# Optimization experiments

Hardware: AMD Instinct MI355X
Metric: run time of the kernel (lower is better)

Reference implementation:

```python
import jax, jax.numpy as jnp
import numpy as np

N, M, D, K = 50000, 32, 128, 8
DELTA_D = D // K
EPS = 1e-12  # torch F.normalize eps


def _normalize(v, axis):
    nrm = jnp.linalg.norm(v, axis=axis, keepdims=True)
    return v / jnp.maximum(nrm, EPS)


def setup_inputs() -> dict:
    key = jax.random.key(0)
    k1, k2 = jax.random.split(key)
    x = jax.random.normal(k1, (N, D), dtype=jnp.float32)
    neighbors = jax.random.randint(k2, (N * M,), 0, N + 1, dtype=jnp.int64)
    return {"x": x, "neighbors": neighbors, "max_iter": 6}


def reference(x, neighbors, max_iter):
    n, d = x.shape
    m = neighbors.shape[0] // n
    k, delta_d = K, DELTA_D
    # per-capsule L2 normalize input features
    x = _normalize(x.reshape(n, k, delta_d), axis=2).reshape(n, d)
    # append zero row for padding index n, gather neighbor features
    z = jnp.concatenate([x, jnp.zeros((1, d), dtype=x.dtype)], axis=0)
    z = z[neighbors].reshape(n, m, k, delta_d)
    x_c = x.reshape(n, k, delta_d)
    u = None
    for it in range(max_iter):
        if u is None:
            p = jnp.zeros((n, m, k), dtype=x.dtype)
        else:
            p = jnp.einsum('nmkd,nkd->nmk', z, u)
        p = jax.nn.softmax(p, axis=2)
        u = jnp.einsum('nmkd,nmk->nkd', z, p) + x_c
        if it < max_iter - 1:
            u = _normalize(u, axis=2)
    return u.reshape(n, d)
```

## Files before the change

### kernel.cpp

```cpp
#include <hip/hip_runtime.h>
#include <math.h>


constexpr int NROWS = 50000;
constexpr int MN = 32;
constexpr int DDIM = 128;
constexpr float FEPS2 = 1e-24f;
constexpr float LOG2E = 1.44269504088896340736f;

#if __has_builtin(__builtin_amdgcn_rcpf)
__device__ __forceinline__ float fast_rcp(float v) { return __builtin_amdgcn_rcpf(v); }
#else
__device__ __forceinline__ float fast_rcp(float v) { return __frcp_rn(v); }
#endif
#if __has_builtin(__builtin_amdgcn_rsqf)
__device__ __forceinline__ float fast_rsq(float v) { return __builtin_amdgcn_rsqf(v); }
#else
__device__ __forceinline__ float fast_rsq(float v) { return rsqrtf(v); }
#endif
#if __has_builtin(__builtin_amdgcn_exp2f)
__device__ __forceinline__ float fast_exp2(float v) { return __builtin_amdgcn_exp2f(v); }
#else
__device__ __forceinline__ float fast_exp2(float v) { return exp2f(v); }
#endif

template <int CTRL>
__device__ __forceinline__ float dpp_add(float v) {
    int r = __builtin_amdgcn_update_dpp(0, __builtin_bit_cast(int, v), CTRL, 0xF, 0xF, true);
    return v + __builtin_bit_cast(float, r);
}

__device__ __forceinline__ void load16(float (&dst)[16], const float* __restrict__ p) {
    const float4* q = reinterpret_cast<const float4*>(p);
#pragma unroll
    for (int i = 0; i < 4; ++i) {
        float4 v = q[i];
        dst[4 * i + 0] = v.x; dst[4 * i + 1] = v.y;
        dst[4 * i + 2] = v.z; dst[4 * i + 3] = v.w;
    }
}

__device__ __forceinline__ void normalize16(float (&v)[16]) {
    float a = v[0] * v[0], b = v[1] * v[1];
#pragma unroll
    for (int d = 2; d < 16; d += 2) {
        a = fmaf(v[d], v[d], a);
        b = fmaf(v[d + 1], v[d + 1], b);
    }
    float iv = fast_rsq(fmaxf(a + b, FEPS2));
#pragma unroll
    for (int d = 0; d < 16; ++d) v[d] *= iv;
}

__device__ __forceinline__ void butterfly8(float (&u)[16]) {
#pragma unroll
    for (int d = 0; d < 16; ++d) u[d] = dpp_add<0xB1>(u[d]);
#pragma unroll
    for (int d = 0; d < 16; ++d) u[d] = dpp_add<0x4E>(u[d]);
#pragma unroll
    for (int d = 0; d < 16; ++d) u[d] += __shfl_xor(u[d], 4);
}

__device__ __forceinline__ float inv_norm_log2e(const float (&u)[16]) {
    float a = u[0] * u[0], b = u[1] * u[1];
#pragma unroll
    for (int d = 2; d < 16; d += 2) {
        a = fmaf(u[d], u[d], a);
        b = fmaf(u[d + 1], u[d + 1], b);
    }
    return fast_rsq(fmaxf(a + b, FEPS2)) * LOG2E;
}

__global__ __launch_bounds__(256) void norm_kernel(const float* __restrict__ x,
                                                   float* __restrict__ xn) {
    int t = blockIdx.x * 256 + threadIdx.x;
    constexpr int TOTAL = (NROWS + 1) * (DDIM / 4);
    if (t >= TOTAL) return;
    int n = t >> 5;
    float4 v = make_float4(0.f, 0.f, 0.f, 0.f);
    if (n < NROWS) v = reinterpret_cast<const float4*>(x)[t];
    float ss = v.x * v.x;
    ss = fmaf(v.y, v.y, ss);
    ss = fmaf(v.z, v.z, ss);
    ss = fmaf(v.w, v.w, ss);
    ss = dpp_add<0xB1>(ss);
    ss = dpp_add<0x4E>(ss);
    float iv = fast_rsq(fmaxf(ss, FEPS2));
    v.x *= iv; v.y *= iv; v.z *= iv; v.w *= iv;
    reinterpret_cast<float4*>(xn)[t] = v;
}

template <bool PRENORM>
__global__ __launch_bounds__(256, 4) void routing_kernel(const float* __restrict__ xsrc,
                                                         const int* __restrict__ nbr,
                                                         float* __restrict__ out) {
    const int lane = threadIdx.x & 63;
    const int n = blockIdx.x * 4 + (threadIdx.x >> 6);
    const int j = lane & 7;
    const int k = lane >> 3;

    float xc8[16];
    load16(xc8, xsrc + n * DDIM + k * 16);
    if (!PRENORM) normalize16(xc8);
#pragma unroll
    for (int d = 0; d < 16; ++d) xc8[d] *= 0.125f;

    float z[4][16];
    {
        const int* __restrict__ nrow = nbr + n * MN;
        int idx[4];
#pragma unroll
        for (int t = 0; t < 4; ++t) idx[t] = nrow[j + 8 * t];
#pragma unroll
        for (int t = 0; t < 4; ++t) {
            if (PRENORM) {
                load16(z[t], xsrc + idx[t] * DDIM + k * 16);
            } else {
                if (idx[t] < NROWS) {
                    load16(z[t], xsrc + idx[t] * DDIM + k * 16);
                    normalize16(z[t]);
                } else {
#pragma unroll
                    for (int d = 0; d < 16; ++d) z[t][d] = 0.f;
                }
            }
        }
    }

    float u[16];
#pragma unroll
    for (int d = 0; d < 16; ++d) {
        float a = fmaf(z[0][d], 0.125f, xc8[d]);
        a = fmaf(z[1][d], 0.125f, a);
        a = fmaf(z[2][d], 0.125f, a);
        a = fmaf(z[3][d], 0.125f, a);
        u[d] = a;
    }
    butterfly8(u);
    float c = inv_norm_log2e(u);

#pragma unroll
    for (int it = 1; it < 6; ++it) {
        float pn[4];
#pragma unroll
        for (int t = 0; t < 4; ++t) {
            float a = z[t][0] * u[0], b = z[t][1] * u[1];
#pragma unroll
            for (int d = 2; d < 16; d += 2) {
                a = fmaf(z[t][d], u[d], a);
                b = fmaf(z[t][d + 1], u[d + 1], b);
            }
            float e = fast_exp2((a + b) * c);
            float s = dpp_add<0x128>(e);
            s += __shfl_xor(s, 16);
            s += __shfl_xor(s, 32);
            pn[t] = e * fast_rcp(s);
        }
#pragma unroll
        for (int d = 0; d < 16; ++d) {
            float a = fmaf(z[0][d], pn[0], xc8[d]);
            a = fmaf(z[1][d], pn[1], a);
            a = fmaf(z[2][d], pn[2], a);
            a = fmaf(z[3][d], pn[3], a);
            u[d] = a;
        }
        butterfly8(u);
        if (it < 5) c = inv_norm_log2e(u);
    }

    float w0 = u[0], w1 = u[1];
#pragma unroll
    for (int d = 1; d < 8; ++d) {
        if (j == d) { w0 = u[2 * d]; w1 = u[2 * d + 1]; }
    }
    *reinterpret_cast<float2*>(out + n * DDIM + 2 * lane) = make_float2(w0, w1);
}

extern "C" void kernel_launch(void* const* d_in, const int* in_sizes, int n_in,
                              void* d_out, int out_size, void* d_ws, size_t ws_size,
                              hipStream_t stream) {
    const float* x = (const float*)d_in[0];
    const int* nbr = (const int*)d_in[1];
    float* out = (float*)d_out;

    const size_t need = (size_t)(NROWS + 1) * DDIM * sizeof(float);
    if (ws_size >= need) {
        float* xn = (float*)d_ws;
        constexpr int TOTAL = (NROWS + 1) * (DDIM / 4);
        norm_kernel<<<(TOTAL + 255) / 256, 256, 0, stream>>>(x, xn);
        routing_kernel<true><<<NROWS / 4, 256, 0, stream>>>(xn, nbr, out);
    } else {
        routing_kernel<false><<<NROWS / 4, 256, 0, stream>>>(x, nbr, out);
    }
}
```

Measured before the change: 203.4 us.

## Store normalized features in fp16 and use packed fp16 dot products

The normalized feature table is now written as fp16, halving the bytes moved by the random neighbor gather. The routing kernel keeps the neighbor vectors in packed half2 registers, computes the agreement dot products with fdot2, and accumulates the weighted sums in fp32. Fewer registers allow the launch-bounds occupancy hint to rise from 4 to 5. The cost is reduced precision in the gathered features and routing logits, which may push results past tolerance.

```diff
diff --git a/kernel.cpp b/kernel.cpp
--- a/kernel.cpp
+++ b/kernel.cpp
@@ -8,6 +8,12 @@
 constexpr float FEPS2 = 1e-24f;
 constexpr float LOG2E = 1.44269504088896340736f;
 
+typedef _Float16 h2 __attribute__((ext_vector_type(2)));
+typedef _Float16 h8 __attribute__((ext_vector_type(8)));
+typedef __fp16 fp16x2 __attribute__((ext_vector_type(2)));
+
+union H8Cast { h8 v; h2 p[4]; };
+
 #if __has_builtin(__builtin_amdgcn_rcpf)
 __device__ __forceinline__ float fast_rcp(float v) { return __builtin_amdgcn_rcpf(v); }
 #else
@@ -30,6 +36,27 @@
     return v + __builtin_bit_cast(float, r);
 }
 
+__device__ __forceinline__ float hdot2(h2 a, h2 b, float c) {
+#if __has_builtin(__builtin_amdgcn_fdot2)
+    return __builtin_amdgcn_fdot2(__builtin_bit_cast(fp16x2, a),
+                                  __builtin_bit_cast(fp16x2, b), c, false);
+#else
+    return fmaf((float)a[0], (float)b[0], fmaf((float)a[1], (float)b[1], c));
+#endif
+}
+
+__device__ __forceinline__ h2 pack2(float a, float b) {
+#if __has_builtin(__builtin_amdgcn_cvt_pkrtz)
+    return __builtin_bit_cast(h2, __builtin_amdgcn_cvt_pkrtz(a, b));
+#else
+    h2 r; r[0] = (_Float16)a; r[1] = (_Float16)b; return r;
+#endif
+}
+
+__device__ __forceinline__ float mixfma(_Float16 h, float s, float acc) {
+    return fmaf((float)h, s, acc);
+}
+
 __device__ __forceinline__ void load16(float (&dst)[16], const float* __restrict__ p) {
     const float4* q = reinterpret_cast<const float4*>(p);
 #pragma unroll
@@ -72,7 +99,7 @@
 }
 
 __global__ __launch_bounds__(256) void norm_kernel(const float* __restrict__ x,
-                                                   float* __restrict__ xn) {
+                                                   _Float16* __restrict__ xn) {
     int t = blockIdx.x * 256 + threadIdx.x;
     constexpr int TOTAL = (NROWS + 1) * (DDIM / 4);
     if (t >= TOTAL) return;
@@ -86,12 +113,16 @@
     ss = dpp_add<0xB1>(ss);
     ss = dpp_add<0x4E>(ss);
     float iv = fast_rsq(fmaxf(ss, FEPS2));
-    v.x *= iv; v.y *= iv; v.z *= iv; v.w *= iv;
-    reinterpret_cast<float4*>(xn)[t] = v;
+    h2 lo = pack2(v.x * iv, v.y * iv);
+    h2 hi = pack2(v.z * iv, v.w * iv);
+    float2 w;
+    w.x = __builtin_bit_cast(float, lo);
+    w.y = __builtin_bit_cast(float, hi);
+    reinterpret_cast<float2*>(xn)[t] = w;
 }
 
 template <bool PRENORM>
-__global__ __launch_bounds__(256, 4) void routing_kernel(const float* __restrict__ xsrc,
+__global__ __launch_bounds__(256, 5) void routing_kernel(const void* __restrict__ xsrc,
                                                          const int* __restrict__ nbr,
                                                          float* __restrict__ out) {
     const int lane = threadIdx.x & 63;
@@ -99,56 +130,83 @@
     const int j = lane & 7;
     const int k = lane >> 3;
 
-    float xc8[16];
-    load16(xc8, xsrc + n * DDIM + k * 16);
-    if (!PRENORM) normalize16(xc8);
-#pragma unroll
-    for (int d = 0; d < 16; ++d) xc8[d] *= 0.125f;
-
-    float z[4][16];
-    {
-        const int* __restrict__ nrow = nbr + n * MN;
-        int idx[4];
-#pragma unroll
-        for (int t = 0; t < 4; ++t) idx[t] = nrow[j + 8 * t];
+    const int* __restrict__ nrow = nbr + n * MN;
+    int idx[4];
+#pragma unroll
+    for (int t = 0; t < 4; ++t) idx[t] = nrow[j + 8 * t];
+
+    h2 z[4][8];
+    h2 xch[8];
+
+    if constexpr (PRENORM) {
+        const _Float16* xh = (const _Float16*)xsrc;
+        {
+            const h8* p = (const h8*)(xh + (size_t)n * DDIM + k * 16);
+            H8Cast a, b; a.v = p[0]; b.v = p[1];
+#pragma unroll
+            for (int q = 0; q < 4; ++q) { xch[q] = a.p[q]; xch[q + 4] = b.p[q]; }
+        }
 #pragma unroll
         for (int t = 0; t < 4; ++t) {
-            if (PRENORM) {
-                load16(z[t], xsrc + idx[t] * DDIM + k * 16);
+            const h8* p = (const h8*)(xh + (size_t)idx[t] * DDIM + k * 16);
+            H8Cast a, b; a.v = p[0]; b.v = p[1];
+#pragma unroll
+            for (int q = 0; q < 4; ++q) { z[t][q] = a.p[q]; z[t][q + 4] = b.p[q]; }
+        }
+    } else {
+        const float* xf = (const float*)xsrc;
+        float tmp[16];
+        load16(tmp, xf + (size_t)n * DDIM + k * 16);
+        normalize16(tmp);
+#pragma unroll
+        for (int q = 0; q < 8; ++q) xch[q] = pack2(tmp[2 * q], tmp[2 * q + 1]);
+#pragma unroll
+        for (int t = 0; t < 4; ++t) {
+            if (idx[t] < NROWS) {
+                load16(tmp, xf + (size_t)idx[t] * DDIM + k * 16);
+                normalize16(tmp);
             } else {
-                if (idx[t] < NROWS) {
-                    load16(z[t], xsrc + idx[t] * DDIM + k * 16);
-                    normalize16(z[t]);
-                } else {
-#pragma unroll
-                    for (int d = 0; d < 16; ++d) z[t][d] = 0.f;
-                }
+#pragma unroll
+                for (int d = 0; d < 16; ++d) tmp[d] = 0.f;
             }
-        }
-    }
+#pragma unroll
+            for (int q = 0; q < 8; ++q) z[t][q] = pack2(tmp[2 * q], tmp[2 * q + 1]);
+        }
+    }
+
+#pragma unroll
+    for (int q = 0; q < 8; ++q) xch[q] = xch[q] * (_Float16)0.125f;
 
     float u[16];
 #pragma unroll
-    for (int d = 0; d < 16; ++d) {
-        float a = fmaf(z[0][d], 0.125f, xc8[d]);
-        a = fmaf(z[1][d], 0.125f, a);
-        a = fmaf(z[2][d], 0.125f, a);
-        a = fmaf(z[3][d], 0.125f, a);
-        u[d] = a;
+    for (int q = 0; q < 8; ++q) {
+#pragma unroll
+        for (int g = 0; g < 2; ++g) {
+            float acc = (float)xch[q][g];
+            acc = mixfma(z[0][q][g], 0.125f, acc);
+            acc = mixfma(z[1][q][g], 0.125f, acc);
+            acc = mixfma(z[2][q][g], 0.125f, acc);
+            acc = mixfma(z[3][q][g], 0.125f, acc);
+            u[2 * q + g] = acc;
+        }
     }
     butterfly8(u);
     float c = inv_norm_log2e(u);
+    h2 uh[8];
+#pragma unroll
+    for (int q = 0; q < 8; ++q) uh[q] = pack2(u[2 * q], u[2 * q + 1]);
 
 #pragma unroll
     for (int it = 1; it < 6; ++it) {
         float pn[4];
 #pragma unroll
         for (int t = 0; t < 4; ++t) {
-            float a = z[t][0] * u[0], b = z[t][1] * u[1];
-#pragma unroll
-            for (int d = 2; d < 16; d += 2) {
-                a = fmaf(z[t][d], u[d], a);
-                b = fmaf(z[t][d + 1], u[d + 1], b);
+            float a = hdot2(z[t][0], uh[0], 0.f);
+            float b = hdot2(z[t][1], uh[1], 0.f);
+#pragma unroll
+            for (int q = 2; q < 8; q += 2) {
+                a = hdot2(z[t][q], uh[q], a);
+                b = hdot2(z[t][q + 1], uh[q + 1], b);
             }
             float e = fast_exp2((a + b) * c);
             float s = dpp_add<0x128>(e);
@@ -157,15 +215,23 @@
             pn[t] = e * fast_rcp(s);
         }
 #pragma unroll
-        for (int d = 0; d < 16; ++d) {
-            float a = fmaf(z[0][d], pn[0], xc8[d]);
-            a = fmaf(z[1][d], pn[1], a);
-            a = fmaf(z[2][d], pn[2], a);
-            a = fmaf(z[3][d], pn[3], a);
-            u[d] = a;
+        for (int q = 0; q < 8; ++q) {
+#pragma unroll
+            for (int g = 0; g < 2; ++g) {
+                float acc = (float)xch[q][g];
+                acc = mixfma(z[0][q][g], pn[0], acc);
+                acc = mixfma(z[1][q][g], pn[1], acc);
+                acc = mixfma(z[2][q][g], pn[2], acc);
+                acc = mixfma(z[3][q][g], pn[3], acc);
+                u[2 * q + g] = acc;
+            }
         }
         butterfly8(u);
-        if (it < 5) c = inv_norm_log2e(u);
+        if (it < 5) {
+            c = inv_norm_log2e(u);
+#pragma unroll
+            for (int q = 0; q < 8; ++q) uh[q] = pack2(u[2 * q], u[2 * q + 1]);
+        }
     }
 
     float w0 = u[0], w1 = u[1];
@@ -173,7 +239,7 @@
     for (int d = 1; d < 8; ++d) {
         if (j == d) { w0 = u[2 * d]; w1 = u[2 * d + 1]; }
     }
-    *reinterpret_cast<float2*>(out + n * DDIM + 2 * lane) = make_float2(w0, w1);
+    *reinterpret_cast<float2*>(out + (size_t)n * DDIM + 2 * lane) = make_float2(w0, w1);
 }
 
 extern "C" void kernel_launch(void* const* d_in, const int* in_sizes, int n_in,
@@ -183,9 +249,9 @@
     const int* nbr = (const int*)d_in[1];
     float* out = (float*)d_out;
 
-    const size_t need = (size_t)(NROWS + 1) * DDIM * sizeof(float);
+    const size_t need = (size_t)(NROWS + 1) * DDIM * sizeof(_Float16);
     if (ws_size >= need) {
-        float* xn = (float*)d_ws;
+        _Float16* xn = (_Float16*)d_ws;
         constexpr int TOTAL = (NROWS + 1) * (DDIM / 4);
         norm_kernel<<<(TOTAL + 255) / 256, 256, 0, stream>>>(x, xn);
         routing_kernel<true><<<NROWS / 4, 256, 0, stream>>>(xn, nbr, out);
```

Result: slower. 777.1 us (+281.9%).
